# Kernel tuning notes

Measured on AMD Instinct MI355X. Metric: run time of the kernel, lower is better.

## Reference

```python
import jax, jax.numpy as jnp
import numpy as np

B, CIN, T = 16, 1, 262144
A = 128            # n_atoms
K = 16             # kernel_size == stride
ITERS = 8          # n_iterations
NCLS = 3           # ternary
EPS = 1e-4


def setup_inputs() -> dict:
    key = jax.random.key(0)
    ks = jax.random.split(key, 10)
    n = lambda k, shape, sc: jax.random.normal(k, shape, dtype=jnp.float32) * sc
    return dict(
        x=jax.random.normal(ks[0], (B, CIN, T), dtype=jnp.float32),
        Wx=n(ks[1], (A, CIN, K), 0.25),      # conv weight, fan_in=16
        bx=n(ks[2], (A,), 0.05),
        Wh=n(ks[3], (A, A), 0.05),           # 1x1 conv, no bias
        Wk=n(ks[4], (A, A), 0.08), bk=n(ks[5], (A,), 0.05),
        Wt=n(ks[6], (A, A), 0.08), bt=n(ks[7], (A,), 0.05),
        Wp=n(ks[8], (A * NCLS, A), 0.08), bp=n(ks[9], (A * NCLS,), 0.05),
    )


def reference(x, Wx, bx, Wh, Wk, bk, Wt, bt, Wp, bp):
    Bsz, C, Tlen = x.shape
    Tp = Tlen // K  # T'
    # stride==kernel conv is a blocked channel matmul
    xr = x.reshape(Bsz, C, Tp, K)
    h_x = jnp.einsum('bctk,ack->bat', xr, Wx) + bx[:, None]  # [B, A, T']

    def step(h, _):
        h = jax.nn.relu(h_x + jnp.einsum('oi,bit->bot', Wh, h))
        return h, None

    h, _ = jax.lax.scan(step, jnp.zeros_like(h_x), None, length=ITERS)

    k_out = jax.nn.softplus(jnp.einsum('oi,bit->bot', Wk, h) + bk[:, None]) + EPS
    theta_out = jax.nn.softplus(jnp.einsum('oi,bit->bot', Wt, h) + bt[:, None]) + EPS
    pi = jnp.einsum('oi,bit->bot', Wp, h) + bp[:, None]        # [B, A*NCLS, T']
    logits = pi.reshape(Bsz, A, NCLS, Tp).transpose(0, 1, 3, 2)  # [B, A, T', NCLS]
    return k_out, theta_out, logits
```

## Files before the change

### kernel.cpp

```cpp
#include <hip/hip_runtime.h>


typedef __attribute__((ext_vector_type(8))) short short8;
typedef __attribute__((ext_vector_type(2))) unsigned uint2v;
typedef __attribute__((ext_vector_type(4))) float float4v;

#define TP 16384
#define THETA_OFF 33554432u
#define LOGIT_OFF 67108864u

#define WS_WXF 16384
#define WS_WCF 20480
#define WS_TOTAL 102400

__device__ __forceinline__ short f2bf(float f) {
  union { float f; unsigned u; } v; v.f = f;
  unsigned r = (v.u + 0x7fffu + ((v.u >> 16) & 1u)) >> 16;
  return (short)r;
}

__device__ __forceinline__ unsigned cvt_pk_bf16(float a, float b) {
  unsigned r;
  asm("v_cvt_pk_bf16_f32 %0, %1, %2" : "=v"(r) : "v"(a), "v"(b));
  return r;
}

__global__ void prep_kernel(const float* __restrict__ Wx, const float* __restrict__ Wh,
                            const float* __restrict__ Wk, const float* __restrict__ Wt,
                            const float* __restrict__ Wp, short* __restrict__ wsbf) {
  int i = blockIdx.x * 256 + threadIdx.x;
  if (i >= WS_TOTAL) return;
  float val;
  if (i < WS_WXF) {
    int e = i, f = e >> 9, lane = (e >> 3) & 63, j = e & 7;
    int mt = f >> 2, ks = f & 3, q = lane >> 4, r = lane & 15;
    val = Wh[(mt * 16 + r) * 128 + ks * 32 + q * 8 + j];
  } else if (i < WS_WCF) {
    int e = i - WS_WXF, mt = e >> 9, lane = (e >> 3) & 63, j = e & 7;
    int q = lane >> 4, r = lane & 15;
    val = (q < 2) ? Wx[(mt * 16 + r) * 16 + q * 8 + j] : 0.0f;
  } else {
    int e = i - WS_WCF, f = e >> 9, lane = (e >> 3) & 63, j = e & 7;
    int rt = f >> 2, ks = f & 3, q = lane >> 4, r = lane & 15;
    int m = rt * 16 + r, k = ks * 32 + q * 8 + j;
    if (rt < 8)       val = Wk[m * 128 + k];
    else if (rt < 16) val = Wt[(m - 128) * 128 + k];
    else              val = Wp[(m - 256) * 128 + k];
  }
  wsbf[i] = f2bf(val);
}

__global__ __launch_bounds__(256, 3) void ista_kernel(
    const float* __restrict__ x,  const float* __restrict__ bx,
    const float* __restrict__ bk, const float* __restrict__ bt,
    const float* __restrict__ bp, const short* __restrict__ wsbf,
    float* __restrict__ out) {
  __shared__ short WhLds[16384];
  __shared__ short Hlds[64 * 136];

  const int tid  = threadIdx.x;
  const int w    = tid >> 6;
  const int lane = tid & 63;
  const int q    = lane >> 4;
  const int r    = lane & 15;
  const int g0   = blockIdx.x << 6;
  const int b    = g0 >> 14;
  const int t0   = g0 & (TP - 1);
  const int col_local = (w << 4) + r;

  {
    const short8* src = (const short8*)wsbf;
    short8* dst = (short8*)WhLds;
#pragma unroll
    for (int k2 = 0; k2 < 8; ++k2) dst[(k2 << 8) + tid] = src[(k2 << 8) + tid];
  }

  short8 xfrag;
  {
    union { short8 s; unsigned u[4]; } xu;
    xu.u[0] = xu.u[1] = xu.u[2] = xu.u[3] = 0u;
    if (q < 2) {
      const float* xp = x + (((size_t)(g0 + col_local)) << 4) + (q << 3);
      xu.u[0] = cvt_pk_bf16(xp[0], xp[1]);
      xu.u[1] = cvt_pk_bf16(xp[2], xp[3]);
      xu.u[2] = cvt_pk_bf16(xp[4], xp[5]);
      xu.u[3] = cvt_pk_bf16(xp[6], xp[7]);
    }
    xfrag = xu.s;
  }

  const short8* wxfp = (const short8*)(wsbf + WS_WXF);
  float4v hx[8];
#pragma unroll
  for (int mt = 0; mt < 8; ++mt) {
    float4v c = *(const float4v*)(bx + (mt << 4) + (q << 2));
    hx[mt] = __builtin_amdgcn_mfma_f32_16x16x32_bf16(wxfp[(mt << 6) + lane], xfrag, c, 0, 0, 0);
  }

  short* hrow = &Hlds[col_local * 136];
#pragma unroll
  for (int mt = 0; mt < 8; ++mt) {
    uint2v v2;
    v2[0] = cvt_pk_bf16(fmaxf(hx[mt][0], 0.0f), fmaxf(hx[mt][1], 0.0f));
    v2[1] = cvt_pk_bf16(fmaxf(hx[mt][2], 0.0f), fmaxf(hx[mt][3], 0.0f));
    *(uint2v*)(hrow + (mt << 4) + (q << 2)) = v2;
  }

  __syncthreads();

  const char* whb = (const char*)WhLds;
  int wboff = lane << 4;
  for (int it = 1; it < 8; ++it) {
    asm("" : "+v"(wboff));
    short8 Bf[4];
#pragma unroll
    for (int ks = 0; ks < 4; ++ks)
      Bf[ks] = *(const short8*)(hrow + (ks << 5) + (q << 3));
#pragma unroll
    for (int mt = 0; mt < 8; ++mt) {
      float4v c = hx[mt];
#pragma unroll
      for (int ks = 0; ks < 4; ++ks) {
        const short8 A = *(const short8*)(whb + ((((mt << 2) + ks) << 10)) + wboff);
        c = __builtin_amdgcn_mfma_f32_16x16x32_bf16(A, Bf[ks], c, 0, 0, 0);
      }
      uint2v v2;
      v2[0] = cvt_pk_bf16(fmaxf(c[0], 0.0f), fmaxf(c[1], 0.0f));
      v2[1] = cvt_pk_bf16(fmaxf(c[2], 0.0f), fmaxf(c[3], 0.0f));
      *(uint2v*)(hrow + (mt << 4) + (q << 2)) = v2;
    }
  }

  __syncthreads();

  short8 Ball[16];
#pragma unroll
  for (int nt = 0; nt < 4; ++nt)
#pragma unroll
    for (int ks = 0; ks < 4; ++ks)
      Ball[(nt << 2) + ks] =
          *(const short8*)&Hlds[((nt << 4) + r) * 136 + (ks << 5) + (q << 3)];

  const short8* wcfp = (const short8*)(wsbf + WS_WCF);
  const size_t brow = ((size_t)b) << 7;

  for (int rti = 0; rti < 10; ++rti) {
    const int rt = (rti << 2) + w;
    short8 Af[4];
#pragma unroll
    for (int ks = 0; ks < 4; ++ks) Af[ks] = wcfp[(((rt << 2) + ks) << 6) + lane];
    const int grb = (rt << 4) + (q << 2);
    float4v bias;
    if (rti < 2)      bias = *(const float4v*)(bk + grb);
    else if (rti < 4) bias = *(const float4v*)(bt + grb - 128);
    else              bias = *(const float4v*)(bp + grb - 256);

#pragma unroll
    for (int nt = 0; nt < 4; ++nt) {
      float4v c = {0.0f, 0.0f, 0.0f, 0.0f};
#pragma unroll
      for (int ks = 0; ks < 4; ++ks)
        c = __builtin_amdgcn_mfma_f32_16x16x32_bf16(Af[ks], Ball[(nt << 2) + ks], c, 0, 0, 0);
      const int t = t0 + (nt << 4) + r;

      if (rti < 4) {
        const size_t off  = (rti < 2) ? (size_t)0 : (size_t)THETA_OFF;
        const int    arow = (rti < 2) ? grb : grb - 128;
        float* po = out + off + ((brow + (size_t)arow) << 14) + (size_t)t;
#pragma unroll
        for (int g = 0; g < 4; ++g) {
          const float v  = c[g] + bias[g];
          const float sp = fmaxf(v, 0.0f) + __logf(1.0f + __expf(-fabsf(v))) + 1e-4f;
          po[(size_t)g << 14] = sp;
        }
      } else {
        const unsigned o0  = (unsigned)(grb - 256);
        const unsigned a0  = o0 / 3u;
        const unsigned rem = o0 - a0 * 3u;
#pragma unroll
        for (int g = 0; g < 4; ++g) {
          const float v = c[g] + bias[g];
          const unsigned cc  = rem + (unsigned)g;
          const unsigned adj = (cc >= 3u) ? 1u : 0u;
          const unsigned a   = a0 + adj;
          const unsigned ci  = cc - adj * 3u;
          out[(size_t)LOGIT_OFF + ((((brow + (size_t)a) << 14) + (size_t)t) * 3u) + ci] = v;
        }
      }
    }
  }
}

extern "C" void kernel_launch(void* const* d_in, const int* in_sizes, int n_in,
                              void* d_out, int out_size, void* d_ws, size_t ws_size,
                              hipStream_t stream) {
  const float* x  = (const float*)d_in[0];
  const float* Wx = (const float*)d_in[1];
  const float* bx = (const float*)d_in[2];
  const float* Wh = (const float*)d_in[3];
  const float* Wk = (const float*)d_in[4];
  const float* bk = (const float*)d_in[5];
  const float* Wt = (const float*)d_in[6];
  const float* bt = (const float*)d_in[7];
  const float* Wp = (const float*)d_in[8];
  const float* bp = (const float*)d_in[9];
  short* wsbf = (short*)d_ws;
  float* out  = (float*)d_out;

  hipLaunchKernelGGL(prep_kernel, dim3(WS_TOTAL / 256), dim3(256), 0, stream,
                     Wx, Wh, Wk, Wt, Wp, wsbf);
  hipLaunchKernelGGL(ista_kernel, dim3(4096), dim3(256), 0, stream,
                     x, bx, bk, bt, bp, wsbf, out);
}
```

Baseline: 739.9 us.

## Keep Wh fragments in registers and split recurrence by output rows across waves

Each wave previously owned 16 time columns and streamed all of Wh from LDS every iteration. Now each wave owns two 16-row output tiles, keeps its Wh fragments in registers, and reads H for all 64 columns from a double-buffered LDS array, with a barrier per iteration. This removes the 32KB Wh LDS copy and its repeated LDS reads, and raises the occupancy hint from 3 to 4 blocks per CU. The cost is seven block-wide barriers per recurrence and more register pressure from the held weight and accumulator fragments.

```diff
diff --git a/kernel.cpp b/kernel.cpp
--- a/kernel.cpp
+++ b/kernel.cpp
@@ -12,6 +12,8 @@
 #define WS_WXF 16384
 #define WS_WCF 20480
 #define WS_TOTAL 102400
+
+#define HSTRIDE 136
 
 __device__ __forceinline__ short f2bf(float f) {
   union { float f; unsigned u; } v; v.f = f;
@@ -50,13 +52,12 @@
   wsbf[i] = f2bf(val);
 }
 
-__global__ __launch_bounds__(256, 3) void ista_kernel(
+__global__ __launch_bounds__(256, 4) void ista_kernel(
     const float* __restrict__ x,  const float* __restrict__ bx,
     const float* __restrict__ bk, const float* __restrict__ bt,
     const float* __restrict__ bp, const short* __restrict__ wsbf,
     float* __restrict__ out) {
-  __shared__ short WhLds[16384];
-  __shared__ short Hlds[64 * 136];
+  __shared__ short Hbuf[2][64 * HSTRIDE];
 
   const int tid  = threadIdx.x;
   const int w    = tid >> 6;
@@ -66,72 +67,86 @@
   const int g0   = blockIdx.x << 6;
   const int b    = g0 >> 14;
   const int t0   = g0 & (TP - 1);
-  const int col_local = (w << 4) + r;
-
-  {
-    const short8* src = (const short8*)wsbf;
-    short8* dst = (short8*)WhLds;
-#pragma unroll
-    for (int k2 = 0; k2 < 8; ++k2) dst[(k2 << 8) + tid] = src[(k2 << 8) + tid];
-  }
-
-  short8 xfrag;
-  {
+  const int mt0  = w << 1;
+  const int mt1  = mt0 + 1;
+
+  const short8* whfp = (const short8*)wsbf;
+  short8 whf0[4], whf1[4];
+#pragma unroll
+  for (int ks = 0; ks < 4; ++ks) {
+    whf0[ks] = whfp[(((mt0 << 2) + ks) << 6) + lane];
+    whf1[ks] = whfp[(((mt1 << 2) + ks) << 6) + lane];
+  }
+
+  short8 xfrag[4];
+#pragma unroll
+  for (int nt = 0; nt < 4; ++nt) {
     union { short8 s; unsigned u[4]; } xu;
     xu.u[0] = xu.u[1] = xu.u[2] = xu.u[3] = 0u;
     if (q < 2) {
-      const float* xp = x + (((size_t)(g0 + col_local)) << 4) + (q << 3);
+      const float* xp = x + (((size_t)(g0 + (nt << 4) + r)) << 4) + (q << 3);
       xu.u[0] = cvt_pk_bf16(xp[0], xp[1]);
       xu.u[1] = cvt_pk_bf16(xp[2], xp[3]);
       xu.u[2] = cvt_pk_bf16(xp[4], xp[5]);
       xu.u[3] = cvt_pk_bf16(xp[6], xp[7]);
     }
-    xfrag = xu.s;
+    xfrag[nt] = xu.s;
   }
 
   const short8* wxfp = (const short8*)(wsbf + WS_WXF);
-  float4v hx[8];
-#pragma unroll
-  for (int mt = 0; mt < 8; ++mt) {
-    float4v c = *(const float4v*)(bx + (mt << 4) + (q << 2));
-    hx[mt] = __builtin_amdgcn_mfma_f32_16x16x32_bf16(wxfp[(mt << 6) + lane], xfrag, c, 0, 0, 0);
-  }
-
-  short* hrow = &Hlds[col_local * 136];
-#pragma unroll
-  for (int mt = 0; mt < 8; ++mt) {
-    uint2v v2;
-    v2[0] = cvt_pk_bf16(fmaxf(hx[mt][0], 0.0f), fmaxf(hx[mt][1], 0.0f));
-    v2[1] = cvt_pk_bf16(fmaxf(hx[mt][2], 0.0f), fmaxf(hx[mt][3], 0.0f));
-    *(uint2v*)(hrow + (mt << 4) + (q << 2)) = v2;
-  }
-
+  const short8 wxf0 = wxfp[(mt0 << 6) + lane];
+  const short8 wxf1 = wxfp[(mt1 << 6) + lane];
+  const float4v bias0 = *(const float4v*)(bx + (mt0 << 4) + (q << 2));
+  const float4v bias1 = *(const float4v*)(bx + (mt1 << 4) + (q << 2));
+  float4v hx0[4], hx1[4];
+#pragma unroll
+  for (int nt = 0; nt < 4; ++nt) {
+    hx0[nt] = __builtin_amdgcn_mfma_f32_16x16x32_bf16(wxf0, xfrag[nt], bias0, 0, 0, 0);
+    hx1[nt] = __builtin_amdgcn_mfma_f32_16x16x32_bf16(wxf1, xfrag[nt], bias1, 0, 0, 0);
+  }
+
+#pragma unroll
+  for (int nt = 0; nt < 4; ++nt) {
+    short* hc = &Hbuf[0][((nt << 4) + r) * HSTRIDE];
+    uint2v v0, v1;
+    v0[0] = cvt_pk_bf16(fmaxf(hx0[nt][0], 0.0f), fmaxf(hx0[nt][1], 0.0f));
+    v0[1] = cvt_pk_bf16(fmaxf(hx0[nt][2], 0.0f), fmaxf(hx0[nt][3], 0.0f));
+    v1[0] = cvt_pk_bf16(fmaxf(hx1[nt][0], 0.0f), fmaxf(hx1[nt][1], 0.0f));
+    v1[1] = cvt_pk_bf16(fmaxf(hx1[nt][2], 0.0f), fmaxf(hx1[nt][3], 0.0f));
+    *(uint2v*)(hc + (mt0 << 4) + (q << 2)) = v0;
+    *(uint2v*)(hc + (mt1 << 4) + (q << 2)) = v1;
+  }
   __syncthreads();
 
-  const char* whb = (const char*)WhLds;
-  int wboff = lane << 4;
+  const short* hr = Hbuf[0];
+  short* hw = Hbuf[1];
+#pragma unroll
   for (int it = 1; it < 8; ++it) {
-    asm("" : "+v"(wboff));
-    short8 Bf[4];
-#pragma unroll
-    for (int ks = 0; ks < 4; ++ks)
-      Bf[ks] = *(const short8*)(hrow + (ks << 5) + (q << 3));
-#pragma unroll
-    for (int mt = 0; mt < 8; ++mt) {
-      float4v c = hx[mt];
+#pragma unroll
+    for (int nt = 0; nt < 4; ++nt) {
+      const short* hcr = hr + ((nt << 4) + r) * HSTRIDE;
+      short8 Bf[4];
+#pragma unroll
+      for (int ks = 0; ks < 4; ++ks)
+        Bf[ks] = *(const short8*)(hcr + (ks << 5) + (q << 3));
+      float4v c0 = hx0[nt], c1 = hx1[nt];
 #pragma unroll
       for (int ks = 0; ks < 4; ++ks) {
-        const short8 A = *(const short8*)(whb + ((((mt << 2) + ks) << 10)) + wboff);
-        c = __builtin_amdgcn_mfma_f32_16x16x32_bf16(A, Bf[ks], c, 0, 0, 0);
+        c0 = __builtin_amdgcn_mfma_f32_16x16x32_bf16(whf0[ks], Bf[ks], c0, 0, 0, 0);
+        c1 = __builtin_amdgcn_mfma_f32_16x16x32_bf16(whf1[ks], Bf[ks], c1, 0, 0, 0);
       }
-      uint2v v2;
-      v2[0] = cvt_pk_bf16(fmaxf(c[0], 0.0f), fmaxf(c[1], 0.0f));
-      v2[1] = cvt_pk_bf16(fmaxf(c[2], 0.0f), fmaxf(c[3], 0.0f));
-      *(uint2v*)(hrow + (mt << 4) + (q << 2)) = v2;
+      short* hcw = hw + ((nt << 4) + r) * HSTRIDE;
+      uint2v v0, v1;
+      v0[0] = cvt_pk_bf16(fmaxf(c0[0], 0.0f), fmaxf(c0[1], 0.0f));
+      v0[1] = cvt_pk_bf16(fmaxf(c0[2], 0.0f), fmaxf(c0[3], 0.0f));
+      v1[0] = cvt_pk_bf16(fmaxf(c1[0], 0.0f), fmaxf(c1[1], 0.0f));
+      v1[1] = cvt_pk_bf16(fmaxf(c1[2], 0.0f), fmaxf(c1[3], 0.0f));
+      *(uint2v*)(hcw + (mt0 << 4) + (q << 2)) = v0;
+      *(uint2v*)(hcw + (mt1 << 4) + (q << 2)) = v1;
     }
-  }
-
-  __syncthreads();
+    __syncthreads();
+    const short* tmp = hr; hr = hw; hw = (short*)tmp;
+  }
 
   short8 Ball[16];
 #pragma unroll
@@ -139,7 +154,7 @@
 #pragma unroll
     for (int ks = 0; ks < 4; ++ks)
       Ball[(nt << 2) + ks] =
-          *(const short8*)&Hlds[((nt << 4) + r) * 136 + (ks << 5) + (q << 3)];
+          *(const short8*)(hr + ((nt << 4) + r) * HSTRIDE + (ks << 5) + (q << 3));
 
   const short8* wcfp = (const short8*)(wsbf + WS_WCF);
   const size_t brow = ((size_t)b) << 7;
```

Result: no change. 748.9 us (+1.2%).
